# Optimization experiments

Hardware: AMD Instinct MI355X
Metric: run time of the kernel (lower is better)

The kernel has to match this reference:

```python
import jax, jax.numpy as jnp
import numpy as np

B = 256
K = 64          # num_walks_per_node
L = 32          # max_walk_len
SENTINEL = L    # unseen-node position sentinel
NUM_SLOTS = 100000  # node-id table size (static stand-in for walks.max()+1)
HALF = 64       # pos_dim // 2


def setup_inputs() -> dict:
    key = jax.random.key(0)
    ks = jax.random.split(key, 6)
    src_walks = jax.random.randint(ks[0], (B, K, L), 0, NUM_SLOTS, dtype=jnp.int32)
    tgt_walks = jax.random.randint(ks[1], (B, K, L), 0, NUM_SLOTS, dtype=jnp.int32)
    src_lens = jax.random.randint(ks[2], (B, K), 0, L + 1, dtype=jnp.int32)
    tgt_lens = jax.random.randint(ks[3], (B, K), 0, L + 1, dtype=jnp.int32)
    own_emb = jax.random.normal(ks[4], (L + 1, HALF), dtype=jnp.float32)
    cross_emb = jax.random.normal(ks[5], (L + 1, HALF), dtype=jnp.float32)
    return {"src_walks": src_walks, "tgt_walks": tgt_walks,
            "src_lens": src_lens, "tgt_lens": tgt_lens,
            "own_emb": own_emb, "cross_emb": cross_emb}


def _valid_mask(walks, lens):
    # (B,K,L) bool: within length and non-padding (node id != 0)
    pos = jnp.arange(walks.shape[-1], dtype=lens.dtype)[None, None, :]
    return (pos < lens[..., None]) & (walks != 0)


def _saw_table(walks, valid):
    # Per-node minimum walk position via scatter-min. (B, NUM_SLOTS) int32.
    b, k, l = walks.shape
    m = k * l
    flat = walks.reshape(b, m)
    pos = jnp.tile(jnp.arange(l, dtype=walks.dtype), k)[None, :]  # (1, M)
    pos = jnp.where(valid.reshape(b, m), pos, SENTINEL)
    pos = jnp.broadcast_to(pos, (b, m))
    table = jnp.full((b, NUM_SLOTS), SENTINEL, dtype=walks.dtype)
    bidx = jnp.arange(b)[:, None]
    return table.at[bidx, flat].min(pos)


def reference(src_walks, tgt_walks, src_lens, tgt_lens, own_emb, cross_emb):
    b, k, l = src_walks.shape
    m = k * l
    src_valid = _valid_mask(src_walks, src_lens)
    tgt_valid = _valid_mask(tgt_walks, tgt_lens)
    src_table = _saw_table(src_walks, src_valid)
    tgt_table = _saw_table(tgt_walks, tgt_valid)

    src_flat = src_walks.reshape(b, m)
    tgt_flat = tgt_walks.reshape(b, m)
    gather = lambda table, flat: jnp.take_along_axis(table, flat, axis=1).reshape(b, k, l)
    src_own = gather(src_table, src_flat)    # own-perspective first-seen pos
    tgt_own = gather(tgt_table, tgt_flat)
    src_cross = gather(tgt_table, src_flat)  # cross-perspective
    tgt_cross = gather(src_table, tgt_flat)

    src_pos = jnp.concatenate([own_emb[src_own], cross_emb[src_cross]], axis=-1)
    tgt_pos = jnp.concatenate([own_emb[tgt_own], cross_emb[tgt_cross]], axis=-1)
    src_pos = src_pos * src_valid[..., None].astype(src_pos.dtype)
    tgt_pos = tgt_pos * tgt_valid[..., None].astype(tgt_pos.dtype)
    return src_pos, tgt_pos
```

## Files before the change

kernel.cpp:

```cpp
#include <hip/hip_runtime.h>
#include <stdint.h>

#define B 256
#define K 64
#define L 32
#define SENTINEL 32u
#define NUM_SLOTS 100000
#define HALF 64


#define HASH_SIZE 4096
#define HASH_MASK 4095u
#define THREADS 1024

typedef float fvec4 __attribute__((ext_vector_type(4)));

__global__ __launch_bounds__(THREADS) void wpe_fused_kernel(
    const int* __restrict__ src_walks,
    const int* __restrict__ tgt_walks,
    const int* __restrict__ src_lens,
    const int* __restrict__ tgt_lens,
    const float* __restrict__ own_emb,
    const float* __restrict__ cross_emb,
    fvec4* __restrict__ out) {
  __shared__ int          s_keys[HASH_SIZE];
  __shared__ unsigned int s_vsrc[HASH_SIZE];
  __shared__ unsigned int s_vtgt[HASH_SIZE];
  __shared__ int          s_lens[2 * K];

  const unsigned int b = blockIdx.x;
  const unsigned int t = threadIdx.x;
  const unsigned int base = b * (K * L);

  for (unsigned int i = t; i < HASH_SIZE; i += THREADS) {
    s_keys[i] = 0;
    s_vsrc[i] = SENTINEL;
    s_vtgt[i] = SENTINEL;
  }
  if (t < 2 * K) {
    s_lens[t] = (t < K) ? src_lens[b * K + t] : tgt_lens[b * K + (t - K)];
  }
  __syncthreads();

  for (unsigned int e = t; e < 2u * K * L; e += THREADS) {
    unsigned int which = e >> 11;
    unsigned int idx   = e & 2047u;
    unsigned int l     = idx & (L - 1);
    unsigned int k     = idx >> 5;
    const int* walks = which ? tgt_walks : src_walks;
    int node = walks[base + idx];
    int len  = s_lens[which * K + k];
    if ((int)l < len && node != 0) {
      unsigned int h = ((unsigned int)node * 0x9E3779B1u) >> 20;
      while (true) {
        int prev = atomicCAS(&s_keys[h], 0, node);
        if (prev == 0 || prev == node) break;
        h = (h + 1) & HASH_MASK;
      }
      if (which) atomicMin(&s_vtgt[h], l);
      else       atomicMin(&s_vsrc[h], l);
    }
  }
  __syncthreads();

  const unsigned int c    = t & 7u;
  const unsigned int rsub = t >> 3;
  for (unsigned int pass = 0; pass < 32; ++pass) {
    unsigned int e     = pass * 128u + rsub;
    unsigned int which = e >> 11;
    unsigned int idx   = e & 2047u;
    unsigned int l     = idx & (L - 1);
    unsigned int k     = idx >> 5;
    const int* walks = which ? tgt_walks : src_walks;
    int node = walks[base + idx];
    int len  = s_lens[which * K + k];

    fvec4 vo0, vo1, vc0, vc1;
    if ((int)l < len && node != 0) {
      unsigned int h = ((unsigned int)node * 0x9E3779B1u) >> 20;
      while (s_keys[h] != node) h = (h + 1) & HASH_MASK;
      unsigned int ps = s_vsrc[h];
      unsigned int pt = s_vtgt[h];
      unsigned int pown   = which ? pt : ps;
      unsigned int pcross = which ? ps : pt;
      const fvec4* eo = (const fvec4*)(own_emb   + pown   * HALF);
      const fvec4* ec = (const fvec4*)(cross_emb + pcross * HALF);
      vo0 = eo[c];
      vo1 = eo[c + 8u];
      vc0 = ec[c];
      vc1 = ec[c + 8u];
    } else {
      vo0 = vo1 = vc0 = vc1 = (fvec4)(0.f, 0.f, 0.f, 0.f);
    }
    unsigned int row  = which * (unsigned int)(B * K * L) + base + idx;
    unsigned int ob   = row * 32u;
    out[ob + c]       = vo0;
    out[ob + 8u + c]  = vo1;
    out[ob + 16u + c] = vc0;
    out[ob + 24u + c] = vc1;
  }
}

extern "C" void kernel_launch(void* const* d_in, const int* in_sizes, int n_in,
                              void* d_out, int out_size, void* d_ws, size_t ws_size,
                              hipStream_t stream) {
  const int*   src_walks = (const int*)d_in[0];
  const int*   tgt_walks = (const int*)d_in[1];
  const int*   src_lens  = (const int*)d_in[2];
  const int*   tgt_lens  = (const int*)d_in[3];
  const float* own_emb   = (const float*)d_in[4];
  const float* cross_emb = (const float*)d_in[5];

  wpe_fused_kernel<<<B, THREADS, 0, stream>>>(
      src_walks, tgt_walks, src_lens, tgt_lens, own_emb, cross_emb,
      (fvec4*)d_out);
}
```

Measured before the change: 552.6 us.

## Split fused kernel into hash-resolve and embedding-expand kernels

The single kernel, which ran only 256 blocks and did both the hash-table resolution and the 1 GiB output write, is split in two. The first kernel resolves the own and cross positions and writes a packed 16-bit code per row to workspace. The second kernel launches many small blocks that expand the codes into the embedding output. The aim is to spread the write-bound expansion across the whole GPU instead of 256 large blocks. The cost is an extra launch plus a small round trip of codes through memory.

```diff
diff --git a/kernel.cpp b/kernel.cpp
--- a/kernel.cpp
+++ b/kernel.cpp
@@ -12,17 +12,17 @@
 #define HASH_SIZE 4096
 #define HASH_MASK 4095u
 #define THREADS 1024
+#define ROWS (2 * B * K * L)
+#define ROWS_PER_BATCH (2 * K * L)
 
 typedef float fvec4 __attribute__((ext_vector_type(4)));
 
-__global__ __launch_bounds__(THREADS) void wpe_fused_kernel(
+__global__ __launch_bounds__(THREADS) void wpe_resolve_kernel(
     const int* __restrict__ src_walks,
     const int* __restrict__ tgt_walks,
     const int* __restrict__ src_lens,
     const int* __restrict__ tgt_lens,
-    const float* __restrict__ own_emb,
-    const float* __restrict__ cross_emb,
-    fvec4* __restrict__ out) {
+    unsigned short* __restrict__ codes) {
   __shared__ int          s_keys[HASH_SIZE];
   __shared__ unsigned int s_vsrc[HASH_SIZE];
   __shared__ unsigned int s_vtgt[HASH_SIZE];
@@ -42,7 +42,7 @@
   }
   __syncthreads();
 
-  for (unsigned int e = t; e < 2u * K * L; e += THREADS) {
+  for (unsigned int e = t; e < ROWS_PER_BATCH; e += THREADS) {
     unsigned int which = e >> 11;
     unsigned int idx   = e & 2047u;
     unsigned int l     = idx & (L - 1);
@@ -63,10 +63,7 @@
   }
   __syncthreads();
 
-  const unsigned int c    = t & 7u;
-  const unsigned int rsub = t >> 3;
-  for (unsigned int pass = 0; pass < 32; ++pass) {
-    unsigned int e     = pass * 128u + rsub;
+  for (unsigned int e = t; e < ROWS_PER_BATCH; e += THREADS) {
     unsigned int which = e >> 11;
     unsigned int idx   = e & 2047u;
     unsigned int l     = idx & (L - 1);
@@ -74,8 +71,7 @@
     const int* walks = which ? tgt_walks : src_walks;
     int node = walks[base + idx];
     int len  = s_lens[which * K + k];
-
-    fvec4 vo0, vo1, vc0, vc1;
+    unsigned short code = 0xFFFFu;
     if ((int)l < len && node != 0) {
       unsigned int h = ((unsigned int)node * 0x9E3779B1u) >> 20;
       while (s_keys[h] != node) h = (h + 1) & HASH_MASK;
@@ -83,22 +79,41 @@
       unsigned int pt = s_vtgt[h];
       unsigned int pown   = which ? pt : ps;
       unsigned int pcross = which ? ps : pt;
-      const fvec4* eo = (const fvec4*)(own_emb   + pown   * HALF);
-      const fvec4* ec = (const fvec4*)(cross_emb + pcross * HALF);
-      vo0 = eo[c];
-      vo1 = eo[c + 8u];
-      vc0 = ec[c];
-      vc1 = ec[c + 8u];
-    } else {
-      vo0 = vo1 = vc0 = vc1 = (fvec4)(0.f, 0.f, 0.f, 0.f);
+      code = (unsigned short)(pown | (pcross << 6));
     }
-    unsigned int row  = which * (unsigned int)(B * K * L) + base + idx;
-    unsigned int ob   = row * 32u;
-    out[ob + c]       = vo0;
-    out[ob + 8u + c]  = vo1;
-    out[ob + 16u + c] = vc0;
-    out[ob + 24u + c] = vc1;
+    codes[which * (unsigned)(B * K * L) + base + idx] = code;
   }
+}
+
+__global__ __launch_bounds__(256) void wpe_expand_kernel(
+    const unsigned short* __restrict__ codes,
+    const float* __restrict__ own_emb,
+    const float* __restrict__ cross_emb,
+    fvec4* __restrict__ out) {
+  unsigned int tid = blockIdx.x * blockDim.x + threadIdx.x;
+  unsigned int row = tid >> 3;
+  unsigned int c   = tid & 7u;
+
+  unsigned int code = codes[row];
+
+  fvec4 vo0, vo1, vc0, vc1;
+  if (code != 0xFFFFu) {
+    unsigned int pown   = code & 63u;
+    unsigned int pcross = (code >> 6) & 63u;
+    const fvec4* eo = (const fvec4*)(own_emb   + pown   * HALF);
+    const fvec4* ec = (const fvec4*)(cross_emb + pcross * HALF);
+    vo0 = eo[c];
+    vo1 = eo[c + 8u];
+    vc0 = ec[c];
+    vc1 = ec[c + 8u];
+  } else {
+    vo0 = vo1 = vc0 = vc1 = (fvec4)(0.f, 0.f, 0.f, 0.f);
+  }
+  unsigned int ob = row * 32u;
+  out[ob + c]       = vo0;
+  out[ob + 8u + c]  = vo1;
+  out[ob + 16u + c] = vc0;
+  out[ob + 24u + c] = vc1;
 }
 
 extern "C" void kernel_launch(void* const* d_in, const int* in_sizes, int n_in,
@@ -111,7 +126,14 @@
   const float* own_emb   = (const float*)d_in[4];
   const float* cross_emb = (const float*)d_in[5];
 
-  wpe_fused_kernel<<<B, THREADS, 0, stream>>>(
-      src_walks, tgt_walks, src_lens, tgt_lens, own_emb, cross_emb,
-      (fvec4*)d_out);
+  unsigned short* codes = (unsigned short*)d_ws;
+
+  wpe_resolve_kernel<<<B, THREADS, 0, stream>>>(
+      src_walks, tgt_walks, src_lens, tgt_lens, codes);
+
+  {
+    const unsigned int total = ROWS * 8u;
+    wpe_expand_kernel<<<total / 256, 256, 0, stream>>>(
+        codes, own_emb, cross_emb, (fvec4*)d_out);
+  }
 }
```

After: 539.7 us. -2.3%, faster.

## Split each batch across eight blocks that each rebuild the hash table

Applied to the files above, without the earlier changes.

Launches B*8 blocks of 256 threads in place of B blocks of 1024. Every block rebuilds the full per-batch hash table redundantly but writes only one eighth of the output rows. A separate lookup phase packs the own and cross positions into a shared 16-bit code per row, and a later phase expands those codes into embedding writes. The aim is more blocks in flight and better CU occupancy on a 256-CU part, at the price of eightfold redundant table construction and walk reads.

```diff
diff --git a/kernel.cpp b/kernel.cpp
--- a/kernel.cpp
+++ b/kernel.cpp
@@ -11,11 +11,14 @@
 
 #define HASH_SIZE 4096
 #define HASH_MASK 4095u
-#define THREADS 1024
+#define THREADS 256
+#define SLICES 8
+#define EPB (2 * K * L)
+#define SLICE_ROWS (EPB / SLICES)
 
 typedef float fvec4 __attribute__((ext_vector_type(4)));
 
-__global__ __launch_bounds__(THREADS) void wpe_fused_kernel(
+__global__ __launch_bounds__(THREADS) void wpe_fused_wide_kernel(
     const int* __restrict__ src_walks,
     const int* __restrict__ tgt_walks,
     const int* __restrict__ src_lens,
@@ -23,13 +26,15 @@
     const float* __restrict__ own_emb,
     const float* __restrict__ cross_emb,
     fvec4* __restrict__ out) {
-  __shared__ int          s_keys[HASH_SIZE];
-  __shared__ unsigned int s_vsrc[HASH_SIZE];
-  __shared__ unsigned int s_vtgt[HASH_SIZE];
-  __shared__ int          s_lens[2 * K];
+  __shared__ int            s_keys[HASH_SIZE];
+  __shared__ unsigned int   s_vsrc[HASH_SIZE];
+  __shared__ unsigned int   s_vtgt[HASH_SIZE];
+  __shared__ int            s_lens[2 * K];
+  __shared__ unsigned short s_code[SLICE_ROWS];
 
-  const unsigned int b = blockIdx.x;
-  const unsigned int t = threadIdx.x;
+  const unsigned int b    = blockIdx.x >> 3;
+  const unsigned int s    = blockIdx.x & 7u;
+  const unsigned int t    = threadIdx.x;
   const unsigned int base = b * (K * L);
 
   for (unsigned int i = t; i < HASH_SIZE; i += THREADS) {
@@ -42,7 +47,7 @@
   }
   __syncthreads();
 
-  for (unsigned int e = t; e < 2u * K * L; e += THREADS) {
+  for (unsigned int e = t; e < EPB; e += THREADS) {
     unsigned int which = e >> 11;
     unsigned int idx   = e & 2047u;
     unsigned int l     = idx & (L - 1);
@@ -63,10 +68,8 @@
   }
   __syncthreads();
 
-  const unsigned int c    = t & 7u;
-  const unsigned int rsub = t >> 3;
-  for (unsigned int pass = 0; pass < 32; ++pass) {
-    unsigned int e     = pass * 128u + rsub;
+  for (unsigned int j = t; j < SLICE_ROWS; j += THREADS) {
+    unsigned int e     = s * SLICE_ROWS + j;
     unsigned int which = e >> 11;
     unsigned int idx   = e & 2047u;
     unsigned int l     = idx & (L - 1);
@@ -74,8 +77,7 @@
     const int* walks = which ? tgt_walks : src_walks;
     int node = walks[base + idx];
     int len  = s_lens[which * K + k];
-
-    fvec4 vo0, vo1, vc0, vc1;
+    unsigned short code = 0xFFFFu;
     if ((int)l < len && node != 0) {
       unsigned int h = ((unsigned int)node * 0x9E3779B1u) >> 20;
       while (s_keys[h] != node) h = (h + 1) & HASH_MASK;
@@ -83,6 +85,25 @@
       unsigned int pt = s_vtgt[h];
       unsigned int pown   = which ? pt : ps;
       unsigned int pcross = which ? ps : pt;
+      code = (unsigned short)(pown | (pcross << 6));
+    }
+    s_code[j] = code;
+  }
+  __syncthreads();
+
+  for (unsigned int it = 0; it < SLICE_ROWS * 8u / THREADS; ++it) {
+    unsigned int id = it * THREADS + t;
+    unsigned int j  = id >> 3;
+    unsigned int c  = id & 7u;
+    unsigned int e     = s * SLICE_ROWS + j;
+    unsigned int which = e >> 11;
+    unsigned int idx   = e & 2047u;
+    unsigned int code  = s_code[j];
+
+    fvec4 vo0, vo1, vc0, vc1;
+    if (code != 0xFFFFu) {
+      unsigned int pown   = code & 63u;
+      unsigned int pcross = (code >> 6) & 63u;
       const fvec4* eo = (const fvec4*)(own_emb   + pown   * HALF);
       const fvec4* ec = (const fvec4*)(cross_emb + pcross * HALF);
       vo0 = eo[c];
@@ -92,8 +113,8 @@
     } else {
       vo0 = vo1 = vc0 = vc1 = (fvec4)(0.f, 0.f, 0.f, 0.f);
     }
-    unsigned int row  = which * (unsigned int)(B * K * L) + base + idx;
-    unsigned int ob   = row * 32u;
+    unsigned int row = which * (unsigned int)(B * K * L) + base + idx;
+    unsigned int ob  = row * 32u;
     out[ob + c]       = vo0;
     out[ob + 8u + c]  = vo1;
     out[ob + 16u + c] = vc0;
@@ -111,7 +132,7 @@
   const float* own_emb   = (const float*)d_in[4];
   const float* cross_emb = (const float*)d_in[5];
 
-  wpe_fused_kernel<<<B, THREADS, 0, stream>>>(
+  wpe_fused_wide_kernel<<<B * SLICES, THREADS, 0, stream>>>(
       src_walks, tgt_walks, src_lens, tgt_lens, own_emb, cross_emb,
       (fvec4*)d_out);
 }
```

After: 564.7 us. 1.02x slower.
